# Kernel tuning notes

Measured on AMD Instinct MI355X. Metric: run time of the kernel, lower is better.

## Reference

```python
import jax, jax.numpy as jnp
import numpy as np

DOF = 69; NL = 6; H = 8; D = 512; DFF = 2048; HD = D // H; B = 8; T = 512


def prelu(x, a):
    return jnp.where(x >= 0, x, a * x)


def layernorm(x, g, b):
    m = jnp.mean(x, axis=-1, keepdims=True)
    v = jnp.var(x, axis=-1, keepdims=True)
    return (x - m) / jnp.sqrt(v + 1e-6) * g + b


def setup_inputs() -> dict:
    key = jax.random.key(0)
    ks = iter(jax.random.split(key, 64))
    def w(shape, s=0.02):
        return jax.random.normal(next(ks), shape, jnp.float32) * s
    return {
        "x": jax.random.normal(next(ks), (B, T, DOF), jnp.float32),
        "mask_in": (jax.random.uniform(next(ks), (B, T, DOF)) > 0.5).astype(jnp.float32),
        "enc_w1": w((2 * DOF, D)), "enc_b1": jnp.zeros((D,)), "enc_a1": jnp.full((1,), 0.25),
        "enc_w2": w((D, D)), "enc_b2": jnp.zeros((D,)), "enc_a2": jnp.full((1,), 0.25),
        "rel_w1": w((1, D)), "rel_b1": jnp.zeros((D,)), "rel_a": jnp.full((1,), 0.25),
        "rel_w2": w((D, HD)), "rel_b2": jnp.zeros((HD,)),
        "ln_g": jnp.ones((D,)), "ln_b": jnp.zeros((D,)),
        "wq": w((NL, D, D)), "bq": jnp.zeros((NL, D)),
        "wk": w((NL, D, D)), "bk": jnp.zeros((NL, D)),
        "wv": w((NL, D, D)), "bv": jnp.zeros((NL, D)),
        "wo": w((NL, D, D)), "bo": jnp.zeros((NL, D)),
        "fw1": w((NL, D, DFF)), "fb1": jnp.zeros((NL, DFF)), "fa": jnp.full((NL, 1), 0.25),
        "fw2": w((NL, DFF, D)), "fb2": jnp.zeros((NL, D)),
        "dec_w1": w((D, D)), "dec_b1": jnp.zeros((D,)), "dec_a": jnp.full((1,), 0.25),
        "dec_w2": w((D, DOF + 4)), "dec_b2": jnp.zeros((DOF + 4,)),
    }


def _forward(x, mask_in, enc_w1, enc_b1, enc_a1, enc_w2, enc_b2, enc_a2,
             rel_w1, rel_b1, rel_a, rel_w2, rel_b2, ln_g, ln_b,
             wq, bq, wk, bk, wv, bv, wo, bo, fw1, fb1, fa, fw2, fb2,
             dec_w1, dec_b1, dec_a, dec_w2, dec_b2):
    Bv, Tv, _ = x.shape
    # encoder: cat(x, mask) -> Linear-PReLU-Linear-PReLU
    h = prelu(jnp.concatenate([x, mask_in], -1) @ enc_w1 + enc_b1, enc_a1)
    h = prelu(h @ enc_w2 + enc_b2, enc_a2)
    # relative position embedding E_rel: (2T-1, head_dim)
    rel_dist = jnp.arange(-Tv + 1, Tv, dtype=x.dtype)[:, None]
    E = prelu(rel_dist @ rel_w1 + rel_b1, rel_a) @ rel_w2 + rel_b2
    # gather index: idx[i, j] = (j - i) + T - 1
    idx = jnp.arange(Tv)[None, :] - jnp.arange(Tv)[:, None] + Tv - 1  # (T, T)
    scale = 1.0 / np.sqrt(HD).astype(np.float32)
    for l in range(wq.shape[0]):
        hn = layernorm(h, ln_g, ln_b)
        q = (hn @ wq[l] + bq[l]).reshape(Bv, Tv, H, HD)
        k = (hn @ wk[l] + bk[l]).reshape(Bv, Tv, H, HD)
        v = (hn @ wv[l] + bv[l]).reshape(Bv, Tv, H, HD)
        qk = jnp.einsum('bihd,bjhd->bhij', q, k)
        qe = jnp.einsum('bihd,rd->bhir', q, E)          # (B,H,T,2T-1)
        srel = jnp.take_along_axis(qe, idx[None, None], axis=-1)  # skew -> (B,H,T,T)
        attn = jax.nn.softmax((qk + srel) * scale, axis=-1)  # additive mask is all zeros
        o = jnp.einsum('bhij,bjhd->bihd', attn, v).reshape(Bv, Tv, -1)
        h = h + (o @ wo[l] + bo[l])
        hn = layernorm(h, ln_g, ln_b)
        h = h + (prelu(hn @ fw1[l] + fb1[l], fa[l]) @ fw2[l] + fb2[l])
    y = prelu(h @ dec_w1 + dec_b1, dec_a) @ dec_w2 + dec_b2
    return y


def reference(x, mask_in, enc_w1, enc_b1, enc_a1, enc_w2, enc_b2, enc_a2,
              rel_w1, rel_b1, rel_a, rel_w2, rel_b2, ln_g, ln_b,
              wq, bq, wk, bk, wv, bv, wo, bo, fw1, fb1, fa, fw2, fb2,
              dec_w1, dec_b1, dec_a, dec_w2, dec_b2):
    y = _forward(x, mask_in, enc_w1, enc_b1, enc_a1, enc_w2, enc_b2, enc_a2,
                 rel_w1, rel_b1, rel_a, rel_w2, rel_b2, ln_g, ln_b,
                 wq, bq, wk, bk, wv, bv, wo, bo, fw1, fb1, fa, fw2, fb2,
                 dec_w1, dec_b1, dec_a, dec_w2, dec_b2)
    return y[..., :DOF], jax.nn.sigmoid(y[..., DOF:])
```

## Files before the change

### kernel.cpp

```cpp
#include <hip/hip_runtime.h>
#include <hip/hip_bf16.h>

#define DOF 69
#define NL 6
#define NH 8
#define DMODEL 512
#define DFF 2048
#define HD 64
#define BB 8
#define TT 512
#define MTOK (BB*TT)
#define EROWS 1040
#define CATP 192
#define QKP 1024

#define E_OFF     4096u
#define H_OFF     (512u*1024u)
#define HN_OFF    (H_OFF + 8u*1024u*1024u)
#define QKV_OFF   (HN_OFF + 4u*1024u*1024u)
#define WT_OFF    (QKV_OFF + 16u*1024u*1024u)
#define LWT_ELEMS 3145728u

typedef const float* fp32p;
typedef __hip_bfloat16 bf16;
typedef const bf16* bf16p;
typedef __attribute__((ext_vector_type(8))) short bf16x8;
typedef __attribute__((ext_vector_type(4))) short s16x4;
typedef __attribute__((ext_vector_type(4))) float f32x4;

typedef __attribute__((address_space(1))) const void as1_cvoid;
typedef __attribute__((address_space(3))) void       as3_void;

__device__ __forceinline__ void gload16(const bf16* g, const bf16* l){
    __builtin_amdgcn_global_load_lds((as1_cvoid*)g, (as3_void*)l, 16, 0, 0);
}

__device__ __forceinline__ float b2f(bf16 x){ return __bfloat162float(x); }

__global__ __launch_bounds__(256)
void k_concat(fp32p x, fp32p mask, bf16* __restrict__ out){
    int idx = blockIdx.x*256 + threadIdx.x;
    if (idx >= MTOK*CATP) return;
    int row = idx / CATP, c = idx - row*CATP;
    float v = 0.f;
    if (c < DOF) v = x[(size_t)row*DOF + c];
    else if (c < 2*DOF) v = mask[(size_t)row*DOF + (c - DOF)];
    out[idx] = __float2bfloat16(v);
}

__global__ __launch_bounds__(256)
void k_cast(const float* __restrict__ in, bf16* __restrict__ out){
    int idx = blockIdx.x*256 + threadIdx.x;
    if (idx >= MTOK*DMODEL) return;
    out[idx] = __float2bfloat16(in[idx]);
}

__global__ __launch_bounds__(256)
void k_wtall(fp32p wq, fp32p wk, fp32p wv, fp32p wo, fp32p fw1, fp32p fw2,
             fp32p enc_w1, fp32p enc_w2, fp32p dec_w1, fp32p dec_w2,
             bf16* __restrict__ lwt, bf16* __restrict__ ed)
{
    __shared__ float s[32][33];
    const int t = blockIdx.x;
    const int c = threadIdx.x & 31, r0 = threadIdx.x >> 5;

    if (t < 18432) {
        const int l = t / 3072, u = t - l*3072;
        bf16* base = lwt + (size_t)l*LWT_ELEMS;
        fp32p src; bf16* dst; int N, ldk, k0, n0;
        if (u < 1024) {
            int seg = u >> 8, local = u & 255;
            N = 512; ldk = 512;
            k0 = (local & 15) * 32; n0 = (local >> 4) * 32;
            size_t oW = (size_t)l*512*512;
            if      (seg == 0) { src = wq + oW; dst = base; }
            else if (seg == 1) { src = wk + oW; dst = base + 262144; }
            else if (seg == 2) { src = wv + oW; dst = base + 524288; }
            else               { src = wo + oW; dst = base + 786432; }
        } else if (u < 2048) {
            int local = u - 1024;
            N = 2048; ldk = 512;
            k0 = (local & 15) * 32; n0 = (local >> 4) * 32;
            src = fw1 + (size_t)l*512*2048; dst = base + 1048576;
        } else {
            int local = u - 2048;
            N = 512; ldk = 2048;
            k0 = (local >> 4) * 32; n0 = (local & 15) * 32;
            src = fw2 + (size_t)l*2048*512; dst = base + 2097152;
        }
        #pragma unroll
        for (int rr = r0; rr < 32; rr += 8)
            s[rr][c] = src[(size_t)(k0+rr)*N + n0 + c];
        __syncthreads();
        #pragma unroll
        for (int rr = r0; rr < 32; rr += 8)
            dst[(size_t)(n0+rr)*ldk + k0 + c] = __float2bfloat16(s[c][rr]);
        return;
    }

    int t2 = t - 18432;
    fp32p src; bf16* dst; int K, N, ldk, k0, n0;
    if (t2 < 96)       { src = enc_w1; dst = ed;          K = 2*DOF; N = 512; ldk = CATP; k0 = (t2 % 6)*32;  n0 = (t2 / 6)*32; }
    else if (t2 < 352) { int lx = t2 - 96;  src = enc_w2; dst = ed + 512*CATP;          K = 512; N = 512; ldk = 512; k0 = (lx & 15)*32; n0 = (lx >> 4)*32; }
    else if (t2 < 608) { int lx = t2 - 352; src = dec_w1; dst = ed + 512*CATP + 262144; K = 512; N = 512; ldk = 512; k0 = (lx & 15)*32; n0 = (lx >> 4)*32; }
    else               { int lx = t2 - 608; src = dec_w2; dst = ed + 512*CATP + 524288; K = 512; N = DOF+4; ldk = 512; k0 = (lx & 15)*32; n0 = (lx >> 4)*32; }
    #pragma unroll
    for (int rr = r0; rr < 32; rr += 8) {
        int k = k0 + rr, n = n0 + c;
        s[rr][c] = (k < K && n < N) ? src[(size_t)k*N + n] : 0.f;
    }
    __syncthreads();
    #pragma unroll
    for (int rr = r0; rr < 32; rr += 8) {
        int n = n0 + rr;
        if (n < N) dst[(size_t)n*ldk + k0 + c] = __float2bfloat16(s[c][rr]);
    }
}

template<int BM, int BN, int PRELU, int RESID, int BIAS, int OUTF32, int SPLITV>
__global__ __launch_bounds__(256)
void k_gemm(bf16p A, int lda,
            bf16p BT, int ldk,
            fp32p bias, fp32p bias2, fp32p bias3, size_t biasoff,
            fp32p alpha, size_t aidx,
            const float* __restrict__ resid,
            void* __restrict__ Cout, int ldc,
            bf16* __restrict__ VTout,
            int M, int N, int K)
{
    constexpr int MF = BM/32;
    constexpr int NF = BN/32;
    constexpr int AI = BM/32;
    constexpr int BI = BN/32;

    __shared__ __attribute__((aligned(16))) bf16 sA[2][BM*64];
    __shared__ __attribute__((aligned(16))) bf16 sB[2][BN*64];

    int bx, by;
    {
        const int gx  = gridDim.x;
        const int nwg = gx * gridDim.y;
        const int bid = blockIdx.y * gx + blockIdx.x;
        const int qq = nwg >> 3, rr = nwg & 7;
        const int xcd = bid & 7, pos = bid >> 3;
        const int nb = (xcd < rr) ? (xcd*(qq+1) + pos) : (rr*(qq+1) + (xcd-rr)*qq + pos);
        bx = nb % gx; by = nb / gx;
    }

    const int tid  = threadIdx.x;
    const int w    = tid >> 6;
    const int lane = tid & 63;
    const int qd   = lane >> 4;
    const int cl   = lane & 15;
    const int wr   = w >> 1;
    const int wc   = w & 1;
    const int bm   = by * BM;
    const int bn   = bx * BN;

    const int ssc = (lane & 7) ^ ((lane >> 3) & 7);

    const bf16* aG = A + (size_t)(bm + w*(BM/4) + (lane >> 3))*lda + ssc*8;
    const bf16* bG[BI];
    #pragma unroll
    for (int i = 0; i < BI; ++i) {
        int rrow = min(bn + w*(BN/4) + i*8 + (lane >> 3), N-1);
        bG[i] = BT + (size_t)rrow*ldk + ssc*8;
    }

    f32x4 acc[MF][NF] = {};

    auto stage = [&](int p, int k0){
        #pragma unroll
        for (int i = 0; i < AI; ++i)
            gload16(aG + (size_t)(i*8)*lda + k0, &sA[p][(w*(BM/4) + i*8)*64]);
        #pragma unroll
        for (int i = 0; i < BI; ++i)
            gload16(bG[i] + k0, &sB[p][(w*(BN/4) + i*8)*64]);
    };

    stage(0, 0);
    int p = 0;
    for (int k0 = 0; k0 < K; k0 += 64) {
        __syncthreads();
        if (k0 + 64 < K) stage(p^1, k0 + 64);
        #pragma unroll
        for (int ks = 0; ks < 2; ++ks) {
            const int rcc = ks*4 + qd;
            bf16x8 aF[MF], bF[NF];
            #pragma unroll
            for (int mt = 0; mt < MF; ++mt) {
                int row = wr*(BM/2) + mt*16 + cl;
                aF[mt] = *(const bf16x8*)(&sA[p][row*64 + ((rcc ^ (cl & 7))*8)]);
            }
            #pragma unroll
            for (int nt = 0; nt < NF; ++nt) {
                int row = wc*(BN/2) + nt*16 + cl;
                bF[nt] = *(const bf16x8*)(&sB[p][row*64 + ((rcc ^ (cl & 7))*8)]);
            }
            #pragma unroll
            for (int mt = 0; mt < MF; ++mt)
                #pragma unroll
                for (int nt = 0; nt < NF; ++nt)
                    acc[mt][nt] = __builtin_amdgcn_mfma_f32_16x16x32_bf16(aF[mt], bF[nt], acc[mt][nt], 0, 0, 0);
        }
        p ^= 1;
    }

    if (SPLITV && bn >= 1024) {
        #pragma unroll
        for (int nt = 0; nt < NF; ++nt) {
            int col = bn + wc*(BN/2) + nt*16 + cl;
            float bv = bias3[biasoff + (col & 511)];
            int hh = (col >> 6) & 7;
            int hd = col & 63;
            #pragma unroll
            for (int mt = 0; mt < MF; ++mt) {
                int row0 = bm + wr*(BM/2) + mt*16 + qd*4;
                int bb = row0 >> 9, t = row0 & 511;
                s16x4 v4;
                #pragma unroll
                for (int r = 0; r < 4; ++r) {
                    bf16 cb = __float2bfloat16(acc[mt][nt][r] + bv);
                    v4[r] = *reinterpret_cast<short*>(&cb);
                }
                *(s16x4*)(VTout + ((size_t)((bb*8 + hh)*64 + hd))*512 + t) = v4;
            }
        }
        return;
    }

    const float alp = PRELU ? alpha[aidx] : 0.f;
    fp32p bsel = bias;
    if (BIAS == 3) bsel = (bn < 512) ? bias : ((bn < 1024) ? bias2 : bias3);
    #pragma unroll
    for (int nt = 0; nt < NF; ++nt) {
        int col = bn + wc*(BN/2) + nt*16 + cl;
        if (col < N) {
            float bv = 0.f;
            if (BIAS == 1) bv = bsel[biasoff + col];
            if (BIAS == 3) bv = bsel[biasoff + (col & 511)];
            #pragma unroll
            for (int mt = 0; mt < MF; ++mt) {
                #pragma unroll
                for (int r = 0; r < 4; ++r) {
                    int row = bm + wr*(BM/2) + mt*16 + qd*4 + r;
                    float c = acc[mt][nt][r] + bv;
                    if (PRELU) c = (c >= 0.f) ? c : alp*c;
                    if (RESID) c += resid[(size_t)row*ldc + col];
                    if (OUTF32) ((float*)Cout)[(size_t)row*ldc + col] = c;
                    else ((bf16*)Cout)[(size_t)row*ldc + col] = __float2bfloat16(c);
                }
            }
        }
    }
}

__global__ __launch_bounds__(256)
void k_layernorm(const float* __restrict__ x, fp32p g, fp32p b, bf16* __restrict__ out){
    __shared__ float part[8];
    const int row = blockIdx.x, tid = threadIdx.x;
    const int w = tid >> 6, lane = tid & 63;
    const float* xr = x + (size_t)row*DMODEL;
    float x0 = xr[tid], x1 = xr[tid+256];
    float s = x0 + x1, s2 = x0*x0 + x1*x1;
    #pragma unroll
    for (int o = 1; o < 64; o <<= 1) {
        s  += __shfl_xor(s,  o);
        s2 += __shfl_xor(s2, o);
    }
    if (lane == 0) { part[w] = s; part[4+w] = s2; }
    __syncthreads();
    float ts  = part[0] + part[1] + part[2] + part[3];
    float ts2 = part[4] + part[5] + part[6] + part[7];
    float mean = ts * (1.f/DMODEL);
    float var  = ts2 * (1.f/DMODEL) - mean*mean;
    float inv  = rsqrtf(var + 1e-6f);
    out[(size_t)row*DMODEL + tid]     = __float2bfloat16((x0 - mean)*inv*g[tid]     + b[tid]);
    out[(size_t)row*DMODEL + tid+256] = __float2bfloat16((x1 - mean)*inv*g[tid+256] + b[tid+256]);
}

__global__ __launch_bounds__(64)
void k_relemb(fp32p w1, fp32p b1, fp32p a, fp32p w2, fp32p b2, bf16* __restrict__ Ebf){
    __shared__ float sH[DMODEL];
    const int r = blockIdx.x, tid = threadIdx.x;
    if (r >= 2*TT - 1) { Ebf[(size_t)r*HD + tid] = __float2bfloat16(0.f); return; }
    const float dist = (float)(r - (TT-1));
    const float al = a[0];
    for (int d = tid; d < DMODEL; d += 64) {
        float hv = dist * w1[d] + b1[d];
        sH[d] = (hv >= 0.f) ? hv : al*hv;
    }
    __syncthreads();
    float acc = b2[tid];
    for (int d = 0; d < DMODEL; ++d) acc += sH[d] * w2[(size_t)d*HD + tid];
    Ebf[(size_t)r*HD + tid] = __float2bfloat16(acc);
}

__global__ __launch_bounds__(512)
void k_attn(bf16p q, bf16p k, bf16p VT, bf16p Ebf, bf16* __restrict__ o, int qp)
{
    __shared__ __attribute__((aligned(16))) bf16 sK[2][64*64];
    __shared__ __attribute__((aligned(16))) bf16 sV[2][64*64];
    __shared__ __attribute__((aligned(16))) bf16 sE[2][208*64];
    __shared__ float sQE[8][16][100];
    __shared__ __attribute__((aligned(16))) bf16 sP[8][16*64];

    const int bid = blockIdx.x;
    const int it2 = bid >> 6;
    const int h   = bid & 7;
    const int b   = (bid >> 3) & 7;
    const int tid = threadIdx.x;
    const int w   = tid >> 6;
    const int lane= tid & 63;
    const int qd  = lane >> 4;
    const int cl  = lane & 15;

    const int I = it2*128 + w*16;
    const size_t bh   = ((size_t)b*TT)*qp + (size_t)h*HD;
    const size_t boff = ((size_t)b*TT)*DMODEL + (size_t)h*HD;

    const int srow = tid >> 3, sch = tid & 7;
    const int ssc  = sch ^ (srow & 7);
    const int ldso = srow*64 + sch*8;
    const bf16* kg = k  + bh + (size_t)srow*qp + ssc*8;
    const bf16* vg = VT + ((size_t)((b*8 + h)*64 + srow))*512 + ssc*8;
    const int ebase0 = 384 - it2*128;

    auto stage = [&](int p, int J){
        gload16(kg + (size_t)J*qp, &sK[p][ldso]);
        gload16(vg + J,            &sV[p][ldso]);
        const bf16* eg = Ebf + (size_t)(J + ebase0 + srow)*HD + ssc*8;
        gload16(eg,          &sE[p][ldso]);
        gload16(eg + 64*HD,  &sE[p][ldso + 64*64]);
        gload16(eg + 128*HD, &sE[p][ldso + 128*64]);
        if (tid < 128) gload16(eg + 192*HD, &sE[p][ldso + 192*64]);
    };

    bf16x8 qa0, qa1, ones;
    {
        const bf16* qrow = q + bh + (size_t)(I + cl)*qp;
        qa0 = *(const bf16x8*)(qrow + qd*8);
        qa1 = *(const bf16x8*)(qrow + 32 + qd*8);
    }
    #pragma unroll
    for (int e = 0; e < 8; ++e) ((short*)&ones)[e] = 0x3F80;

    f32x4 Oacc[4] = {};
    float m_i[4], l_i[4];
    #pragma unroll
    for (int r = 0; r < 4; ++r) { m_i[r] = -1e30f; l_i[r] = 0.f; }
    const float scale = 0.125f;

    const int c0 = (qd ^ (cl & 7))*8;
    const int c1 = ((qd ^ (cl & 7)) ^ 4)*8;
    const int erow0 = 112 - w*16;

    stage(0, 0);
    int p = 0;

    for (int J = 0; J < TT; J += 64) {
        __syncthreads();
        if (J + 64 < TT) stage(p^1, J + 64);

        f32x4 S[4];
        #pragma unroll
        for (int js = 0; js < 4; ++js) {
            const bf16* kr = &sK[p][(js*16 + cl)*64];
            bf16x8 kb0 = *(const bf16x8*)(kr + c0);
            bf16x8 kb1 = *(const bf16x8*)(kr + c1);
            f32x4 acc = {};
            acc = __builtin_amdgcn_mfma_f32_16x16x32_bf16(qa0, kb0, acc, 0, 0, 0);
            acc = __builtin_amdgcn_mfma_f32_16x16x32_bf16(qa1, kb1, acc, 0, 0, 0);
            S[js] = acc;
        }

        #pragma unroll
        for (int nt = 0; nt < 6; ++nt) {
            const bf16* er = &sE[p][(erow0 + nt*16 + cl)*64];
            bf16x8 eb0 = *(const bf16x8*)(er + c0);
            bf16x8 eb1 = *(const bf16x8*)(er + c1);
            f32x4 acc = {};
            acc = __builtin_amdgcn_mfma_f32_16x16x32_bf16(qa0, eb0, acc, 0, 0, 0);
            acc = __builtin_amdgcn_mfma_f32_16x16x32_bf16(qa1, eb1, acc, 0, 0, 0);
            #pragma unroll
            for (int r = 0; r < 4; ++r)
                sQE[w][qd*4 + r][nt*16 + cl] = acc[r];
        }

        float mnew[4];
        #pragma unroll
        for (int r = 0; r < 4; ++r) mnew[r] = m_i[r];
        #pragma unroll
        for (int js = 0; js < 4; ++js) {
            #pragma unroll
            for (int r = 0; r < 4; ++r) {
                int idx = js*16 + cl - (qd*4 + r) + 15;
                float s = S[js][r] + sQE[w][qd*4 + r][idx];
                S[js][r] = s;
                mnew[r] = fmaxf(mnew[r], s);
            }
        }
        #pragma unroll
        for (int r = 0; r < 4; ++r) {
            float mv = mnew[r];
            mv = fmaxf(mv, __shfl_xor(mv, 1));
            mv = fmaxf(mv, __shfl_xor(mv, 2));
            mv = fmaxf(mv, __shfl_xor(mv, 4));
            mv = fmaxf(mv, __shfl_xor(mv, 8));
            mnew[r] = mv;
        }
        float alpha[4];
        #pragma unroll
        for (int r = 0; r < 4; ++r) {
            alpha[r] = __expf((m_i[r] - mnew[r]) * scale);
            m_i[r] = mnew[r];
        }
        #pragma unroll
        for (int js = 0; js < 4; ++js) {
            #pragma unroll
            for (int r = 0; r < 4; ++r) {
                float pv = __expf((S[js][r] - m_i[r]) * scale);
                int prow = qd*4 + r;
                int pcol = ((js*2 + (cl >> 3)) ^ (prow & 7))*8 + (cl & 7);
                sP[w][prow*64 + pcol] = __float2bfloat16(pv);
            }
        }

        bf16x8 pa0, pa1;
        {
            const bf16* pb = &sP[w][cl*64];
            pa0 = *(const bf16x8*)(pb + c0);
            pa1 = *(const bf16x8*)(pb + c1);
        }

        {
            f32x4 lacc = {};
            lacc = __builtin_amdgcn_mfma_f32_16x16x32_bf16(pa0, ones, lacc, 0, 0, 0);
            lacc = __builtin_amdgcn_mfma_f32_16x16x32_bf16(pa1, ones, lacc, 0, 0, 0);
            #pragma unroll
            for (int r = 0; r < 4; ++r) l_i[r] = l_i[r]*alpha[r] + lacc[r];
        }

        #pragma unroll
        for (int nt = 0; nt < 4; ++nt) {
            #pragma unroll
            for (int r = 0; r < 4; ++r) Oacc[nt][r] *= alpha[r];
            const bf16* vr = &sV[p][(nt*16 + cl)*64];
            bf16x8 vb0 = *(const bf16x8*)(vr + c0);
            bf16x8 vb1 = *(const bf16x8*)(vr + c1);
            Oacc[nt] = __builtin_amdgcn_mfma_f32_16x16x32_bf16(pa0, vb0, Oacc[nt], 0, 0, 0);
            Oacc[nt] = __builtin_amdgcn_mfma_f32_16x16x32_bf16(pa1, vb1, Oacc[nt], 0, 0, 0);
        }
        p ^= 1;
    }

    #pragma unroll
    for (int nt = 0; nt < 4; ++nt) {
        #pragma unroll
        for (int r = 0; r < 4; ++r) {
            int row = qd*4 + r;
            float val = Oacc[nt][r] / l_i[r];
            o[boff + (size_t)(I + row)*DMODEL + nt*16 + cl] = __float2bfloat16(val);
        }
    }
}

__global__ __launch_bounds__(256)
void k_out(const float* __restrict__ y, float* __restrict__ out){
    int idx = blockIdx.x*256 + threadIdx.x;
    if (idx >= MTOK*73) return;
    int row = idx / 73, c = idx - row*73;
    float val = y[idx];
    if (c < DOF) out[(size_t)row*DOF + c] = val;
    else out[(size_t)MTOK*DOF + row*4 + (c-DOF)] = 1.f/(1.f + expf(-val));
}

extern "C" void kernel_launch(void* const* d_in, const int* in_sizes, int n_in,
                              void* d_out, int out_size, void* d_ws, size_t ws_size,
                              hipStream_t stream)
{
    fp32p x      = (fp32p)d_in[0];
    fp32p mask   = (fp32p)d_in[1];
    fp32p enc_w1 = (fp32p)d_in[2];
    fp32p enc_b1 = (fp32p)d_in[3];
    fp32p enc_a1 = (fp32p)d_in[4];
    fp32p enc_w2 = (fp32p)d_in[5];
    fp32p enc_b2 = (fp32p)d_in[6];
    fp32p enc_a2 = (fp32p)d_in[7];
    fp32p rel_w1 = (fp32p)d_in[8];
    fp32p rel_b1 = (fp32p)d_in[9];
    fp32p rel_a  = (fp32p)d_in[10];
    fp32p rel_w2 = (fp32p)d_in[11];
    fp32p rel_b2 = (fp32p)d_in[12];
    fp32p ln_g   = (fp32p)d_in[13];
    fp32p ln_b   = (fp32p)d_in[14];
    fp32p wq     = (fp32p)d_in[15];
    fp32p bq     = (fp32p)d_in[16];
    fp32p wk     = (fp32p)d_in[17];
    fp32p bk     = (fp32p)d_in[18];
    fp32p wv     = (fp32p)d_in[19];
    fp32p bv     = (fp32p)d_in[20];
    fp32p wo     = (fp32p)d_in[21];
    fp32p bo     = (fp32p)d_in[22];
    fp32p fw1    = (fp32p)d_in[23];
    fp32p fb1    = (fp32p)d_in[24];
    fp32p fa     = (fp32p)d_in[25];
    fp32p fw2    = (fp32p)d_in[26];
    fp32p fb2    = (fp32p)d_in[27];
    fp32p dec_w1 = (fp32p)d_in[28];
    fp32p dec_b1 = (fp32p)d_in[29];
    fp32p dec_a  = (fp32p)d_in[30];
    fp32p dec_w2 = (fp32p)d_in[31];
    fp32p dec_b2 = (fp32p)d_in[32];

    char* wsb = (char*)d_ws;
    bf16*  Ebf  = (bf16*)(wsb + E_OFF);
    float* h    = (float*)(wsb + H_OFF);
    bf16*  hn   = (bf16*)(wsb + HN_OFF);
    bf16*  qkb  = (bf16*)(wsb + QKV_OFF);
    bf16*  VTb  = qkb + (size_t)MTOK*QKP;
    bf16*  mid  = qkb;
    bf16*  cat  = qkb;
    bf16*  hb   = qkb;
    float* y    = (float*)qkb;

    bf16* lwt = (bf16*)(wsb + WT_OFF);
    bf16* ed  = lwt + 6*LWT_ELEMS;
    bf16* enc1T = ed;
    bf16* enc2T = ed + 512*CATP;
    bf16* dec1T = enc2T + 262144;
    bf16* dec2T = dec1T + 262144;

    dim3 g512(8, 64);
    dim3 gQKV(12, 64);
    dim3 gF1(16, 64);

    k_wtall<<<19088, 256, 0, stream>>>(wq, wk, wv, wo, fw1, fw2,
                                       enc_w1, enc_w2, dec_w1, dec_w2, lwt, ed);
    k_concat<<<(MTOK*CATP+255)/256, 256, 0, stream>>>(x, mask, cat);
    k_gemm<64,64,1,0,1,0,0><<<g512,256,0,stream>>>(cat, CATP, enc1T, CATP, enc_b1, nullptr, nullptr, 0, enc_a1, 0, nullptr, hn, DMODEL, nullptr, MTOK, DMODEL, CATP);
    k_gemm<64,64,1,0,1,1,0><<<g512,256,0,stream>>>(hn, DMODEL, enc2T, DMODEL, enc_b2, nullptr, nullptr, 0, enc_a2, 0, nullptr, h, DMODEL, nullptr, MTOK, DMODEL, DMODEL);
    k_relemb<<<EROWS, 64, 0, stream>>>(rel_w1, rel_b1, rel_a, rel_w2, rel_b2, Ebf);

    for (int l = 0; l < NL; ++l) {
        size_t oB  = (size_t)l*DMODEL;
        size_t oBF1= (size_t)l*DFF;
        bf16* Lw = lwt + (size_t)l*LWT_ELEMS;

        k_layernorm<<<MTOK, 256, 0, stream>>>(h, ln_g, ln_b, hn);
        k_gemm<64,128,0,0,3,0,1><<<gQKV,256,0,stream>>>(hn, DMODEL, Lw, DMODEL, bq, bk, bv, oB, nullptr, 0, nullptr, qkb, QKP, VTb, MTOK, 1536, DMODEL);
        k_attn<<<BB*NH*(TT/128), 512, 0, stream>>>(qkb, qkb + 512, VTb, Ebf, hn, QKP);
        k_gemm<64,64,0,1,1,1,0><<<g512,256,0,stream>>>(hn, DMODEL, Lw + 786432, DMODEL, bo, nullptr, nullptr, oB, nullptr, 0, h, h, DMODEL, nullptr, MTOK, DMODEL, DMODEL);
        k_layernorm<<<MTOK, 256, 0, stream>>>(h, ln_g, ln_b, hn);
        k_gemm<64,128,1,0,1,0,0><<<gF1,256,0,stream>>>(hn, DMODEL, Lw + 1048576, DMODEL, fb1, nullptr, nullptr, oBF1, fa, (size_t)l, nullptr, mid, DFF, nullptr, MTOK, DFF, DMODEL);
        k_gemm<64,64,0,1,1,1,0><<<g512,256,0,stream>>>(mid, DFF, Lw + 2097152, DFF, fb2, nullptr, nullptr, oB, nullptr, 0, h, h, DMODEL, nullptr, MTOK, DMODEL, DFF);
    }

    k_cast<<<(MTOK*DMODEL+255)/256, 256, 0, stream>>>(h, hb);
    k_gemm<64,64,1,0,1,0,0><<<g512,256,0,stream>>>(hb, DMODEL, dec1T, DMODEL, dec_b1, nullptr, nullptr, 0, dec_a, 0, nullptr, hn, DMODEL, nullptr, MTOK, DMODEL, DMODEL);
    {
        dim3 g2(2, 64);
        k_gemm<64,64,0,0,1,1,0><<<g2,256,0,stream>>>(hn, DMODEL, dec2T, DMODEL, dec_b2, nullptr, nullptr, 0, nullptr, 0, nullptr, y, DOF+4, nullptr, MTOK, DOF+4, DMODEL);
    }
    k_out<<<(MTOK*73+255)/256, 256, 0, stream>>>(y, (float*)d_out);
}
```

Before: 845.9 us.

## Vectorize weight transpose with 64x64 tiles and tighten GEMM prefetch waits

The weight transpose/cast kernel now uses 64x64 tiles with float4 loads and packed 8-wide bf16 stores, cutting the block count and the number of memory transactions. The GEMM main loop swaps __syncthreads for explicit barriers plus s_waitcnt vmcnt(NLD), so the next stage's global loads can stay in flight while the current tile is consumed. It also raises wave priority around the MFMA block. The risk is correctness: the vmcnt count must match the number of outstanding loads, or the code will read shared memory too early.

```diff
diff --git a/kernel.cpp b/kernel.cpp
--- a/kernel.cpp
+++ b/kernel.cpp
@@ -60,60 +60,73 @@
              fp32p enc_w1, fp32p enc_w2, fp32p dec_w1, fp32p dec_w2,
              bf16* __restrict__ lwt, bf16* __restrict__ ed)
 {
-    __shared__ float s[32][33];
+    __shared__ float s[64][65];
     const int t = blockIdx.x;
-    const int c = threadIdx.x & 31, r0 = threadIdx.x >> 5;
-
-    if (t < 18432) {
-        const int l = t / 3072, u = t - l*3072;
+    const int tid = threadIdx.x;
+
+    if (t < 4608) {
+        const int l = t / 768, u = t - l*768;
         bf16* base = lwt + (size_t)l*LWT_ELEMS;
         fp32p src; bf16* dst; int N, ldk, k0, n0;
-        if (u < 1024) {
-            int seg = u >> 8, local = u & 255;
+        if (u < 256) {
+            int seg = u >> 6, local = u & 63;
             N = 512; ldk = 512;
-            k0 = (local & 15) * 32; n0 = (local >> 4) * 32;
+            k0 = (local & 7) * 64; n0 = (local >> 3) * 64;
             size_t oW = (size_t)l*512*512;
             if      (seg == 0) { src = wq + oW; dst = base; }
             else if (seg == 1) { src = wk + oW; dst = base + 262144; }
             else if (seg == 2) { src = wv + oW; dst = base + 524288; }
             else               { src = wo + oW; dst = base + 786432; }
-        } else if (u < 2048) {
-            int local = u - 1024;
+        } else if (u < 512) {
+            int local = u - 256;
             N = 2048; ldk = 512;
-            k0 = (local & 15) * 32; n0 = (local >> 4) * 32;
+            k0 = (local & 7) * 64; n0 = (local >> 3) * 64;
             src = fw1 + (size_t)l*512*2048; dst = base + 1048576;
         } else {
-            int local = u - 2048;
+            int local = u - 512;
             N = 512; ldk = 2048;
-            k0 = (local >> 4) * 32; n0 = (local & 15) * 32;
+            k0 = (local >> 3) * 64; n0 = (local & 7) * 64;
             src = fw2 + (size_t)l*2048*512; dst = base + 2097152;
         }
         #pragma unroll
-        for (int rr = r0; rr < 32; rr += 8)
-            s[rr][c] = src[(size_t)(k0+rr)*N + n0 + c];
+        for (int j = 0; j < 4; ++j) {
+            int idx = j*256 + tid;
+            int row = idx >> 4, cq = idx & 15;
+            float4 v = *(const float4*)(src + (size_t)(k0+row)*N + n0 + cq*4);
+            s[row][cq*4+0] = v.x; s[row][cq*4+1] = v.y;
+            s[row][cq*4+2] = v.z; s[row][cq*4+3] = v.w;
+        }
         __syncthreads();
         #pragma unroll
-        for (int rr = r0; rr < 32; rr += 8)
-            dst[(size_t)(n0+rr)*ldk + k0 + c] = __float2bfloat16(s[c][rr]);
+        for (int j = 0; j < 2; ++j) {
+            int idx = j*256 + tid;
+            int n = idx >> 3, oct = idx & 7;
+            bf16x8 pack;
+            #pragma unroll
+            for (int e = 0; e < 8; ++e) {
+                bf16 cb = __float2bfloat16(s[oct*8 + e][n]);
+                ((short*)&pack)[e] = *reinterpret_cast<short*>(&cb);
+            }
+            *(bf16x8*)(dst + (size_t)(n0+n)*ldk + k0 + oct*8) = pack;
+        }
         return;
     }
 
-    int t2 = t - 18432;
+    int t2 = t - 4608;
     fp32p src; bf16* dst; int K, N, ldk, k0, n0;
-    if (t2 < 96)       { src = enc_w1; dst = ed;          K = 2*DOF; N = 512; ldk = CATP; k0 = (t2 % 6)*32;  n0 = (t2 / 6)*32; }
-    else if (t2 < 352) { int lx = t2 - 96;  src = enc_w2; dst = ed + 512*CATP;          K = 512; N = 512; ldk = 512; k0 = (lx & 15)*32; n0 = (lx >> 4)*32; }
-    else if (t2 < 608) { int lx = t2 - 352; src = dec_w1; dst = ed + 512*CATP + 262144; K = 512; N = 512; ldk = 512; k0 = (lx & 15)*32; n0 = (lx >> 4)*32; }
-    else               { int lx = t2 - 608; src = dec_w2; dst = ed + 512*CATP + 524288; K = 512; N = DOF+4; ldk = 512; k0 = (lx & 15)*32; n0 = (lx >> 4)*32; }
-    #pragma unroll
-    for (int rr = r0; rr < 32; rr += 8) {
-        int k = k0 + rr, n = n0 + c;
-        s[rr][c] = (k < K && n < N) ? src[(size_t)k*N + n] : 0.f;
+    if (t2 < 24)       { src = enc_w1; dst = ed;          K = 2*DOF; N = 512; ldk = CATP; k0 = (t2 % 3)*64; n0 = (t2 / 3)*64; }
+    else if (t2 < 88)  { int lx = t2 - 24;  src = enc_w2; dst = ed + 512*CATP;          K = 512; N = 512;   ldk = 512; k0 = (lx & 7)*64; n0 = (lx >> 3)*64; }
+    else if (t2 < 152) { int lx = t2 - 88;  src = dec_w1; dst = ed + 512*CATP + 262144; K = 512; N = 512;   ldk = 512; k0 = (lx & 7)*64; n0 = (lx >> 3)*64; }
+    else               { int lx = t2 - 152; src = dec_w2; dst = ed + 512*CATP + 524288; K = 512; N = DOF+4; ldk = 512; k0 = (lx >> 1)*64; n0 = (lx & 1)*64; }
+    for (int idx = tid; idx < 4096; idx += 256) {
+        int row = idx >> 6, c = idx & 63;
+        int k = k0 + row, n = n0 + c;
+        s[row][c] = (k < K && n < N) ? src[(size_t)k*N + n] : 0.f;
     }
     __syncthreads();
-    #pragma unroll
-    for (int rr = r0; rr < 32; rr += 8) {
-        int n = n0 + rr;
-        if (n < N) dst[(size_t)n*ldk + k0 + c] = __float2bfloat16(s[c][rr]);
+    for (int idx = tid; idx < 4096; idx += 256) {
+        int n = idx >> 6, c = idx & 63;
+        if (n0 + n < N) dst[(size_t)(n0+n)*ldk + k0 + c] = __float2bfloat16(s[c][n]);
     }
 }
 
@@ -132,6 +145,7 @@
     constexpr int NF = BN/32;
     constexpr int AI = BM/32;
     constexpr int BI = BN/32;
+    constexpr int NLD = AI + BI;
 
     __shared__ __attribute__((aligned(16))) bf16 sA[2][BM*64];
     __shared__ __attribute__((aligned(16))) bf16 sB[2][BN*64];
@@ -181,8 +195,16 @@
     stage(0, 0);
     int p = 0;
     for (int k0 = 0; k0 < K; k0 += 64) {
-        __syncthreads();
-        if (k0 + 64 < K) stage(p^1, k0 + 64);
+        __builtin_amdgcn_s_barrier();
+        if (k0 + 64 < K) {
+            stage(p^1, k0 + 64);
+            asm volatile("s_waitcnt vmcnt(%0)" :: "i"(NLD) : "memory");
+        } else {
+            asm volatile("s_waitcnt vmcnt(0)" ::: "memory");
+        }
+        __builtin_amdgcn_s_barrier();
+        __builtin_amdgcn_sched_barrier(0);
+        __builtin_amdgcn_s_setprio(1);
         #pragma unroll
         for (int ks = 0; ks < 2; ++ks) {
             const int rcc = ks*4 + qd;
@@ -203,6 +225,7 @@
                 for (int nt = 0; nt < NF; ++nt)
                     acc[mt][nt] = __builtin_amdgcn_mfma_f32_16x16x32_bf16(aF[mt], bF[nt], acc[mt][nt], 0, 0, 0);
         }
+        __builtin_amdgcn_s_setprio(0);
         p ^= 1;
     }
 
@@ -535,8 +558,8 @@
     dim3 gQKV(12, 64);
     dim3 gF1(16, 64);
 
-    k_wtall<<<19088, 256, 0, stream>>>(wq, wk, wv, wo, fw1, fw2,
-                                       enc_w1, enc_w2, dec_w1, dec_w2, lwt, ed);
+    k_wtall<<<4776, 256, 0, stream>>>(wq, wk, wv, wo, fw1, fw2,
+                                      enc_w1, enc_w2, dec_w1, dec_w2, lwt, ed);
     k_concat<<<(MTOK*CATP+255)/256, 256, 0, stream>>>(x, mask, cat);
     k_gemm<64,64,1,0,1,0,0><<<g512,256,0,stream>>>(cat, CATP, enc1T, CATP, enc_b1, nullptr, nullptr, 0, enc_a1, 0, nullptr, hn, DMODEL, nullptr, MTOK, DMODEL, CATP);
     k_gemm<64,64,1,0,1,1,0><<<g512,256,0,stream>>>(hn, DMODEL, enc2T, DMODEL, enc_b2, nullptr, nullptr, 0, enc_a2, 0, nullptr, h, DMODEL, nullptr, MTOK, DMODEL, DMODEL);
```

Result: no change. 847.7 us (+0.2%).
